# Kernel tuning notes

Hardware: AMD Instinct MI355X
Metric: run time of the kernel (lower is better)

## Reference

```python
import jax, jax.numpy as jnp
import numpy as np

N, E = 100000, 3200000
IN, HID, OUT, EDGE = 32, 32, 32, 8

def _lin(k, fi, fo):
    s = 1.0 / np.sqrt(fi)
    return jax.random.uniform(k, (fi, fo), jnp.float32, -s, s)

def setup_inputs() -> dict:
    key = jax.random.key(0)
    ks = jax.random.split(key, 12)
    return {
        "node_feat": jax.random.normal(ks[0], (N, IN), jnp.float32),
        "coord_feat": jax.random.normal(ks[1], (N, 3), jnp.float32),
        "edge_feat": jax.random.normal(ks[2], (E, EDGE), jnp.float32),
        "src": jax.random.randint(ks[3], (E,), 0, N, jnp.int32),
        "dst": jax.random.randint(ks[4], (E,), 0, N, jnp.int32),
        # edge MLP: Linear(2*IN+EDGE+1 -> HID), SiLU, Linear(HID -> HID), SiLU
        "We1": _lin(ks[5], 2 * IN + EDGE + 1, HID), "be1": jnp.zeros((HID,), jnp.float32),
        "We2": _lin(ks[6], HID, HID), "be2": jnp.zeros((HID,), jnp.float32),
        # node MLP: Linear(IN+HID -> HID), SiLU, Linear(HID -> OUT)
        "Wn1": _lin(ks[7], IN + HID, HID), "bn1": jnp.zeros((HID,), jnp.float32),
        "Wn2": _lin(ks[8], HID, OUT), "bn2": jnp.zeros((OUT,), jnp.float32),
        # coord MLP: Linear(HID -> HID), SiLU, Linear(HID -> 1, bias=False)
        "Wc1": _lin(ks[9], HID, HID), "bc1": jnp.zeros((HID,), jnp.float32),
        "Wc2": _lin(ks[10], HID, 1),
    }

def reference(node_feat, coord_feat, edge_feat, src, dst,
              We1, be1, We2, be2, Wn1, bn1, Wn2, bn2, Wc1, bc1, Wc2):
    silu = jax.nn.silu
    # per-edge coordinate difference and radial feature (DGL EGNNConv math)
    x_diff = coord_feat[src] - coord_feat[dst]                       # [E,3]
    radial = jnp.sum(x_diff * x_diff, axis=-1, keepdims=True)        # [E,1]
    x_diff = x_diff / (jnp.sqrt(radial) + 1e-30)                     # normalized
    # edge MLP on concat(src_h, dst_h, radial, edge_feat)
    f = jnp.concatenate([node_feat[src], node_feat[dst], radial, edge_feat], axis=-1)
    msg_h = silu(silu(f @ We1 + be1) @ We2 + be2)                    # [E,HID]
    # coordinate message (coord MLP scalar gate * normalized diff)
    msg_x = (silu(msg_h @ Wc1 + bc1) @ Wc2) * x_diff                 # [E,3]
    # aggregate: sum for h messages, mean for coord messages (at dst)
    h_neigh = jax.ops.segment_sum(msg_h, dst, num_segments=N)        # [N,HID]
    deg = jax.ops.segment_sum(jnp.ones((E, 1), msg_x.dtype), dst, num_segments=N)
    x_neigh = jax.ops.segment_sum(msg_x, dst, num_segments=N) / jnp.maximum(deg, 1.0)
    # node update
    h = silu(jnp.concatenate([node_feat, h_neigh], axis=-1) @ Wn1 + bn1) @ Wn2 + bn2
    x = coord_feat + x_neigh
    return h, x
```

## Files before the change

kernel.cpp:

```cpp
#include <hip/hip_runtime.h>
#include <math.h>

#define TIN   32
#define THID  32
#define TOUT  32
#define TEDGE 8
#define CHUNK 4
#define MAXDEG 64
#define OVF_CAP 65536

typedef __attribute__((ext_vector_type(8))) short bf16x8;
typedef __attribute__((ext_vector_type(4))) float f32x4;

#define MFMA16(a, b, c) __builtin_amdgcn_mfma_f32_16x16x32_bf16((a), (b), (c), 0, 0, 0)

__device__ __forceinline__ unsigned int cvtpk(float lo, float hi) {
    unsigned int r;
    asm("v_cvt_pk_bf16_f32 %0, %1, %2" : "=v"(r) : "v"(lo), "v"(hi));
    return r;
}

__device__ __forceinline__ float silu_f(float x) {
    float e = __expf(-x);
    return x * __builtin_amdgcn_rcpf(1.0f + e);
}

__device__ __forceinline__ float bflo(unsigned int u) { return __uint_as_float(u << 16); }
__device__ __forceinline__ float bfhi(unsigned int u) { return __uint_as_float(u & 0xFFFF0000u); }

union U4F { unsigned int u[4]; bf16x8 v; };
union U4Q { uint4 q; bf16x8 v; };

__device__ __forceinline__ bf16x8 pack8bf(const float* f) {
    U4F t;
    t.u[0] = cvtpk(f[0], f[1]);
    t.u[1] = cvtpk(f[2], f[3]);
    t.u[2] = cvtpk(f[4], f[5]);
    t.u[3] = cvtpk(f[6], f[7]);
    return t.v;
}

__device__ __forceinline__ bf16x8 load_wT(const float* __restrict__ W, int kbase, int ch, int Kreal) {
    float f[8];
    #pragma unroll
    for (int e = 0; e < 8; ++e) {
        int k = kbase + e;
        f[e] = (k < Kreal) ? W[k * 32 + ch] : 0.0f;
    }
    return pack8bf(f);
}

__device__ __forceinline__ bf16x8 load_wA12(const float* __restrict__ We1,
                                            const float* __restrict__ be1, int g, int ch) {
    float f[8];
    #pragma unroll
    for (int e = 0; e < 8; ++e) f[e] = 0.0f;
    if (g == 0) { f[0] = We1[72 * 32 + ch]; f[1] = be1[ch]; }
    else if (g == 1) {
        #pragma unroll
        for (int e = 0; e < 8; ++e) f[e] = We1[(64 + e) * 32 + ch];
    }
    return pack8bf(f);
}

__global__ __launch_bounds__(256) void conv_node_kernel(
    const float* __restrict__ nf, unsigned int* __restrict__ nb, int total )
{
    int i = blockIdx.x * 256 + threadIdx.x;
    int stride = gridDim.x * 256;
    for (; i < total; i += stride) {
        float2 v = reinterpret_cast<const float2*>(nf)[i];
        nb[i] = cvtpk(v.x, v.y);
    }
}

__global__ __launch_bounds__(256) void conv_coord_kernel(
    const float* __restrict__ c, float4* __restrict__ c4, int N)
{
    int i = blockIdx.x * 256 + threadIdx.x;
    int stride = gridDim.x * 256;
    for (; i < N; i += stride) {
        float4 v;
        v.x = c[3*(size_t)i+0]; v.y = c[3*(size_t)i+1]; v.z = c[3*(size_t)i+2]; v.w = 0.0f;
        c4[i] = v;
    }
}

__global__ __launch_bounds__(256) void record_rank_kernel(
    const int* __restrict__ src,
    const int* __restrict__ dst,
    const float4* __restrict__ coord4,
    const float* __restrict__ edge_feat,
    int* __restrict__ cnt,
    int* __restrict__ ovf,
    uint4* __restrict__ recs,
    int E)
{
    int e = blockIdx.x * 256 + threadIdx.x;
    if (e >= E) return;
    int s = src[e], d = dst[e];
    int rank = atomicAdd(&cnt[d], 1);
    if (rank >= MAXDEG) {
        int o = atomicAdd(&cnt[ (int)0] + 0, 0);
        (void)o;
        int oi = atomicAdd(ovf - 1 + 1 + OVF_CAP, 0);
        (void)oi;
    }
    if (rank < MAXDEG) {
        float4 cs = coord4[s];
        float4 cd = coord4[d];
        float dx0 = cs.x - cd.x, dx1 = cs.y - cd.y, dx2 = cs.z - cd.z;
        float radial = dx0*dx0 + dx1*dx1 + dx2*dx2;
        float invn = __builtin_amdgcn_rcpf(sqrtf(radial) + 1e-30f);
        dx0 *= invn; dx1 *= invn; dx2 *= invn;

        const float4* ep = reinterpret_cast<const float4*>(edge_feat + (size_t)e * TEDGE);
        float4 e0 = ep[0], e1 = ep[1];

        size_t slot = ((size_t)d << 6) + rank;
        uint4 r0, r1;
        r0.x = (unsigned int)s;
        r0.y = cvtpk(dx0, dx1);
        r0.z = cvtpk(dx2, e1.w);
        r0.w = 0u;
        r1.x = cvtpk(radial, e0.x);
        r1.y = cvtpk(e0.y, e0.z);
        r1.z = cvtpk(e0.w, e1.x);
        r1.w = cvtpk(e1.y, e1.z);
        recs[2*slot + 0] = r0;
        recs[2*slot + 1] = r1;
    } else {
        int oi = atomicAdd(&((int*)cnt)[  0 ], 0);
        (void)oi;
    }
}

__global__ __launch_bounds__(256) void noop_kernel(int x) { (void)x; }

__global__ __launch_bounds__(256) void egnn_fused(
    const uint4* __restrict__ node_bf4,
    const uint4* __restrict__ recs,
    const int*  __restrict__ cnt,
    const float* __restrict__ We1,
    const float* __restrict__ be1,
    const float* __restrict__ We2,
    const float* __restrict__ be2,
    const float* __restrict__ Wc1,
    const float* __restrict__ bc1,
    const float* __restrict__ Wc2,
    float4* __restrict__ h_acc4,
    float4* __restrict__ xd4,
    int N)
{
    const int lane = threadIdx.x & 63;
    const int wid  = threadIdx.x >> 6;
    const int r    = lane & 15;
    const int g    = lane >> 4;

    bf16x8 A10[2], A11[2], A12[2], A2[2], A3[2];
    A10[0] = load_wT(We1,      8*g, r,      73);
    A10[1] = load_wT(We1,      8*g, 16 + r, 73);
    A11[0] = load_wT(We1, 32 + 8*g, r,      73);
    A11[1] = load_wT(We1, 32 + 8*g, 16 + r, 73);
    A12[0] = load_wA12(We1, be1, g, r);
    A12[1] = load_wA12(We1, be1, g, 16 + r);
    A2[0] = load_wT(We2, 8*g, r, 32);      A2[1] = load_wT(We2, 8*g, 16 + r, 32);
    A3[0] = load_wT(Wc1, 8*g, r, 32);      A3[1] = load_wT(Wc1, 8*g, 16 + r, 32);

    float be2v[8], bc1v[8], wc2v[8];
    #pragma unroll
    for (int h = 0; h < 2; ++h)
        #pragma unroll
        for (int q = 0; q < 4; ++q) {
            int ch = 16*h + 4*g + q;
            be2v[4*h+q] = be2[ch];
            bc1v[4*h+q] = bc1[ch];
            wc2v[4*h+q] = Wc2[ch];
        }

    const bool Hhi = ((g >> 1) & 1) != 0;
    const int  s0L = 32 * (g & 1) + r;
    const int  s1L = s0L + 16;

    int c0n = (blockIdx.x * 4 + wid) * CHUNK;

    for (int n = c0n; n < c0n + CHUNK && n < N; ++n) {
        int deg = cnt[n];
        int len = deg < MAXDEG ? deg : MAXDEG;
        size_t segbase = ((size_t)n << 6);

        U4Q Bd; Bd.q = node_bf4[(size_t)n * 4 + g];

        float ha0[4] = {0.f,0.f,0.f,0.f}, ha1[4] = {0.f,0.f,0.f,0.f};
        float xa0 = 0.f, xa1 = 0.f, xa2 = 0.f;

        for (int t = 0; t < len; t += 16) {
            int idx = t + r;
            bool valid = idx < len;
            size_t slot = segbase + (valid ? idx : 0);

            uint4 rc = recs[2*slot + (g & 1)];
            int srcv = __shfl((int)rc.x, r, 64);

            U4Q Bs; Bs.q = node_bf4[(size_t)srcv * 4 + g];

            U4F Bk2;
            Bk2.u[0] = 0u; Bk2.u[1] = 0u; Bk2.u[2] = 0u; Bk2.u[3] = 0u;
            if (g == 0) {
                Bk2.u[0] = (rc.z >> 16) | 0x3F800000u;
            } else if (g == 1) {
                Bk2.u[0] = rc.x; Bk2.u[1] = rc.y; Bk2.u[2] = rc.z; Bk2.u[3] = rc.w;
            }

            f32x4 acc0 = {0.f,0.f,0.f,0.f}, acc1 = {0.f,0.f,0.f,0.f};
            acc0 = MFMA16(A10[0], Bs.v,   acc0);
            acc0 = MFMA16(A11[0], Bd.v,   acc0);
            acc0 = MFMA16(A12[0], Bk2.v,  acc0);
            acc1 = MFMA16(A10[1], Bs.v,   acc1);
            acc1 = MFMA16(A11[1], Bd.v,   acc1);
            acc1 = MFMA16(A12[1], Bk2.v,  acc1);

            unsigned int pk0 = cvtpk(silu_f(acc0[0]), silu_f(acc0[1]));
            unsigned int pk1 = cvtpk(silu_f(acc0[2]), silu_f(acc0[3]));
            unsigned int pk2 = cvtpk(silu_f(acc1[0]), silu_f(acc1[1]));
            unsigned int pk3 = cvtpk(silu_f(acc1[2]), silu_f(acc1[3]));

            unsigned int al0 = __shfl(pk0, s0L, 64), al1 = __shfl(pk1, s0L, 64);
            unsigned int ah0 = __shfl(pk2, s0L, 64), ah1 = __shfl(pk3, s0L, 64);
            unsigned int bl0 = __shfl(pk0, s1L, 64), bl1 = __shfl(pk1, s1L, 64);
            unsigned int bh0 = __shfl(pk2, s1L, 64), bh1 = __shfl(pk3, s1L, 64);
            U4F B2u;
            B2u.u[0] = Hhi ? ah0 : al0;  B2u.u[1] = Hhi ? ah1 : al1;
            B2u.u[2] = Hhi ? bh0 : bl0;  B2u.u[3] = Hhi ? bh1 : bl1;

            f32x4 m0, m1;
            #pragma unroll
            for (int q = 0; q < 4; ++q) { m0[q] = be2v[q]; m1[q] = be2v[4+q]; }
            m0 = MFMA16(A2[0], B2u.v, m0);
            m1 = MFMA16(A2[1], B2u.v, m1);

            float vm = valid ? 1.0f : 0.0f;
            float s00 = silu_f(m0[0]) * vm, s01 = silu_f(m0[1]) * vm;
            float s02 = silu_f(m0[2]) * vm, s03 = silu_f(m0[3]) * vm;
            float s10 = silu_f(m1[0]) * vm, s11 = silu_f(m1[1]) * vm;
            float s12 = silu_f(m1[2]) * vm, s13 = silu_f(m1[3]) * vm;

            ha0[0] += s00; ha0[1] += s01; ha0[2] += s02; ha0[3] += s03;
            ha1[0] += s10; ha1[1] += s11; ha1[2] += s12; ha1[3] += s13;

            unsigned int mpk0 = cvtpk(s00, s01);
            unsigned int mpk1 = cvtpk(s02, s03);
            unsigned int mpk2 = cvtpk(s10, s11);
            unsigned int mpk3 = cvtpk(s12, s13);

            unsigned int cl0 = __shfl(mpk0, s0L, 64), cl1 = __shfl(mpk1, s0L, 64);
            unsigned int ch0 = __shfl(mpk2, s0L, 64), ch1 = __shfl(mpk3, s0L, 64);
            unsigned int dl0 = __shfl(mpk0, s1L, 64), dl1 = __shfl(mpk1, s1L, 64);
            unsigned int dh0 = __shfl(mpk2, s1L, 64), dh1 = __shfl(mpk3, s1L, 64);
            U4F B3u;
            B3u.u[0] = Hhi ? ch0 : cl0;  B3u.u[1] = Hhi ? ch1 : cl1;
            B3u.u[2] = Hhi ? dh0 : dl0;  B3u.u[3] = Hhi ? dh1 : dl1;

            f32x4 c0, c1;
            #pragma unroll
            for (int q = 0; q < 4; ++q) { c0[q] = bc1v[q]; c1[q] = bc1v[4+q]; }
            c0 = MFMA16(A3[0], B3u.v, c0);
            c1 = MFMA16(A3[1], B3u.v, c1);

            float gp = 0.0f;
            #pragma unroll
            for (int q = 0; q < 4; ++q) {
                gp = fmaf(silu_f(c0[q]), wc2v[q],   gp);
                gp = fmaf(silu_f(c1[q]), wc2v[4+q], gp);
            }
            gp += __shfl_xor(gp, 16, 64);
            gp += __shfl_xor(gp, 32, 64);

            float xd0 = bflo(rc.y), xd1 = bfhi(rc.y), xd2 = bflo(rc.z);
            xa0 = fmaf(gp * vm, xd0, xa0);
            xa1 = fmaf(gp * vm, xd1, xa1);
            xa2 = fmaf(gp * vm, xd2, xa2);
        }

        #pragma unroll
        for (int off = 1; off < 16; off <<= 1) {
            #pragma unroll
            for (int q = 0; q < 4; ++q) {
                ha0[q] += __shfl_xor(ha0[q], off, 64);
                ha1[q] += __shfl_xor(ha1[q], off, 64);
            }
            xa0 += __shfl_xor(xa0, off, 64);
            xa1 += __shfl_xor(xa1, off, 64);
            xa2 += __shfl_xor(xa2, off, 64);
        }

        if (r == 0) {
            float4 v0; v0.x = ha0[0]; v0.y = ha0[1]; v0.z = ha0[2]; v0.w = ha0[3];
            float4 v1; v1.x = ha1[0]; v1.y = ha1[1]; v1.z = ha1[2]; v1.w = ha1[3];
            h_acc4[(size_t)n * 8 + g]     = v0;
            h_acc4[(size_t)n * 8 + 4 + g] = v1;
            if (g == 0) {
                float4 xv; xv.x = xa0; xv.y = xa1; xv.z = xa2; xv.w = (float)deg;
                xd4[n] = xv;
            }
        }
    }
}

__global__ __launch_bounds__(256) void ovf_scan_kernel(
    const int* __restrict__ dst, const int* __restrict__ cnt,
    int* __restrict__ ovf_cnt, int* __restrict__ ovf, int E)
{
    int e = blockIdx.x * 256 + threadIdx.x;
    int stride = gridDim.x * 256;
    for (; e < E; e += stride) {
        if (cnt[dst[e]] > MAXDEG) {
            int o = atomicAdd(ovf_cnt, 1);
            if (o < OVF_CAP) ovf[o] = e;
        }
    }
}

__global__ __launch_bounds__(64) void ovf_fix_kernel(
    const float* __restrict__ node_feat,
    const float* __restrict__ coord,
    const float* __restrict__ edge_feat,
    const int* __restrict__ src,
    const int* __restrict__ dst,
    const int* __restrict__ ovf_cnt,
    const int* __restrict__ ovf,
    const float* __restrict__ We1,
    const float* __restrict__ be1,
    const float* __restrict__ We2,
    const float* __restrict__ be2,
    const float* __restrict__ Wc1,
    const float* __restrict__ bc1,
    const float* __restrict__ Wc2,
    float* __restrict__ h_acc,
    float4* __restrict__ xd4,
    int E)
{
    int total = *ovf_cnt;
    if (total > OVF_CAP) total = OVF_CAP;
    for (int i = blockIdx.x * 64 + threadIdx.x; i < total; i += gridDim.x * 64) {
        int e = ovf[i];
        int s = src[e], d = dst[e];
        bool first = true;
        for (int j = 0; j < i; ++j) if (dst[ovf[j]] == d) { first = false; break; }
        if (!first) continue;
        float hsum[THID];
        #pragma unroll
        for (int j = 0; j < THID; ++j) hsum[j] = 0.f;
        float xs0 = 0.f, xs1 = 0.f, xs2 = 0.f;
        int degc = 0;
        for (int ee = 0; ee < E; ++ee) {
            if (dst[ee] != d) continue;
            ++degc;
            int ss = src[ee];
            float dx0 = coord[3*(size_t)ss+0] - coord[3*(size_t)d+0];
            float dx1 = coord[3*(size_t)ss+1] - coord[3*(size_t)d+1];
            float dx2 = coord[3*(size_t)ss+2] - coord[3*(size_t)d+2];
            float radial = dx0*dx0 + dx1*dx1 + dx2*dx2;
            float invn = 1.0f / (sqrtf(radial) + 1e-30f);
            dx0 *= invn; dx1 *= invn; dx2 *= invn;
            float f[73];
            for (int k = 0; k < 32; ++k) f[k] = node_feat[(size_t)ss*TIN + k];
            for (int k = 0; k < 32; ++k) f[32+k] = node_feat[(size_t)d*TIN + k];
            f[64] = radial;
            for (int k = 0; k < 8; ++k) f[65+k] = edge_feat[(size_t)ee*TEDGE + k];
            float a1[THID];
            for (int j = 0; j < THID; ++j) a1[j] = be1[j];
            for (int k = 0; k < 73; ++k) {
                float fk = f[k];
                for (int j = 0; j < THID; ++j) a1[j] = fmaf(fk, We1[k*THID + j], a1[j]);
            }
            for (int j = 0; j < THID; ++j) a1[j] = silu_f(a1[j]);
            float msg[THID];
            for (int j = 0; j < THID; ++j) msg[j] = be2[j];
            for (int k = 0; k < THID; ++k) {
                float fk = a1[k];
                for (int j = 0; j < THID; ++j) msg[j] = fmaf(fk, We2[k*THID + j], msg[j]);
            }
            for (int j = 0; j < THID; ++j) msg[j] = silu_f(msg[j]);
            float c1[THID];
            for (int j = 0; j < THID; ++j) c1[j] = bc1[j];
            for (int k = 0; k < THID; ++k) {
                float fk = msg[k];
                for (int j = 0; j < THID; ++j) c1[j] = fmaf(fk, Wc1[k*THID + j], c1[j]);
            }
            float gate = 0.0f;
            for (int j = 0; j < THID; ++j) gate = fmaf(silu_f(c1[j]), Wc2[j], gate);
            for (int j = 0; j < THID; ++j) hsum[j] += msg[j];
            xs0 += gate * dx0; xs1 += gate * dx1; xs2 += gate * dx2;
        }
        for (int j = 0; j < THID; ++j) h_acc[(size_t)d * THID + j] = hsum[j];
        float4 xv; xv.x = xs0; xv.y = xs1; xv.z = xs2; xv.w = (float)degc;
        xd4[d] = xv;
    }
}

__global__ __launch_bounds__(256) void egnn_edge_atomic(
    const float* __restrict__ node_feat,
    const float* __restrict__ coord,
    const float* __restrict__ edge_feat,
    const int*   __restrict__ src,
    const int*   __restrict__ dst,
    const float* __restrict__ We1,
    const float* __restrict__ be1,
    const float* __restrict__ We2,
    const float* __restrict__ be2,
    const float* __restrict__ Wc1,
    const float* __restrict__ bc1,
    const float* __restrict__ Wc2,
    float* __restrict__ h_acc,
    float* __restrict__ x_acc,
    int E)
{
    int e = blockIdx.x * 256 + threadIdx.x;
    if (e >= E) return;
    int s = src[e];
    int d = dst[e];
    float dx0 = coord[3*(size_t)s+0] - coord[3*(size_t)d+0];
    float dx1 = coord[3*(size_t)s+1] - coord[3*(size_t)d+1];
    float dx2 = coord[3*(size_t)s+2] - coord[3*(size_t)d+2];
    float radial = dx0*dx0 + dx1*dx1 + dx2*dx2;
    float invn = 1.0f / (sqrtf(radial) + 1e-30f);
    dx0 *= invn; dx1 *= invn; dx2 *= invn;
    float f[73];
    #pragma unroll
    for (int i = 0; i < 32; ++i) f[i] = node_feat[(size_t)s*TIN + i];
    #pragma unroll
    for (int i = 0; i < 32; ++i) f[32+i] = node_feat[(size_t)d*TIN + i];
    f[64] = radial;
    #pragma unroll
    for (int i = 0; i < 8; ++i) f[65+i] = edge_feat[(size_t)e*TEDGE + i];
    float a1[THID];
    #pragma unroll
    for (int j = 0; j < THID; ++j) a1[j] = be1[j];
    for (int k = 0; k < 73; ++k) {
        float fk = f[k];
        #pragma unroll
        for (int j = 0; j < THID; ++j) a1[j] = fmaf(fk, We1[k*THID + j], a1[j]);
    }
    #pragma unroll
    for (int j = 0; j < THID; ++j) a1[j] = silu_f(a1[j]);
    float msg[THID];
    #pragma unroll
    for (int j = 0; j < THID; ++j) msg[j] = be2[j];
    for (int k = 0; k < THID; ++k) {
        float fk = a1[k];
        #pragma unroll
        for (int j = 0; j < THID; ++j) msg[j] = fmaf(fk, We2[k*THID + j], msg[j]);
    }
    #pragma unroll
    for (int j = 0; j < THID; ++j) msg[j] = silu_f(msg[j]);
    float c1[THID];
    #pragma unroll
    for (int j = 0; j < THID; ++j) c1[j] = bc1[j];
    for (int k = 0; k < THID; ++k) {
        float fk = msg[k];
        #pragma unroll
        for (int j = 0; j < THID; ++j) c1[j] = fmaf(fk, Wc1[k*THID + j], c1[j]);
    }
    float gate = 0.0f;
    #pragma unroll
    for (int j = 0; j < THID; ++j) gate = fmaf(silu_f(c1[j]), Wc2[j], gate);
    float* ha = h_acc + (size_t)d * THID;
    #pragma unroll
    for (int j = 0; j < THID; ++j) atomicAdd(ha + j, msg[j]);
    atomicAdd(x_acc + (size_t)d*4 + 0, gate * dx0);
    atomicAdd(x_acc + (size_t)d*4 + 1, gate * dx1);
    atomicAdd(x_acc + (size_t)d*4 + 2, gate * dx2);
    atomicAdd(x_acc + (size_t)d*4 + 3, 1.0f);
}

__global__ __launch_bounds__(256) void egnn_node(
    const float* __restrict__ node_feat,
    const float* __restrict__ coord,
    const float* __restrict__ Wn1,
    const float* __restrict__ bn1,
    const float* __restrict__ Wn2,
    const float* __restrict__ bn2,
    const float* __restrict__ h_acc,
    const float4* __restrict__ xd4,
    float* __restrict__ out_h,
    float* __restrict__ out_x,
    int N)
{
    int n = blockIdx.x * 256 + threadIdx.x;
    if (n >= N) return;

    float f2[2*TIN];
    {
        const float4* p = reinterpret_cast<const float4*>(node_feat + (size_t)n * TIN);
        #pragma unroll
        for (int i = 0; i < TIN/4; ++i) {
            float4 v = p[i];
            f2[4*i+0]=v.x; f2[4*i+1]=v.y; f2[4*i+2]=v.z; f2[4*i+3]=v.w;
        }
    }
    {
        const float4* p = reinterpret_cast<const float4*>(h_acc + (size_t)n * THID);
        #pragma unroll
        for (int i = 0; i < THID/4; ++i) {
            float4 v = p[i];
            f2[TIN+4*i+0]=v.x; f2[TIN+4*i+1]=v.y; f2[TIN+4*i+2]=v.z; f2[TIN+4*i+3]=v.w;
        }
    }

    float a[THID];
    #pragma unroll
    for (int j = 0; j < THID; ++j) a[j] = bn1[j];
    #pragma unroll
    for (int k = 0; k < 2*TIN; ++k) {
        float fk = f2[k];
        #pragma unroll
        for (int j = 0; j < THID; ++j) a[j] = fmaf(fk, Wn1[k*THID + j], a[j]);
    }
    #pragma unroll
    for (int j = 0; j < THID; ++j) a[j] = silu_f(a[j]);

    float h[TOUT];
    #pragma unroll
    for (int j = 0; j < TOUT; ++j) h[j] = bn2[j];
    #pragma unroll
    for (int k = 0; k < THID; ++k) {
        float fk = a[k];
        #pragma unroll
        for (int j = 0; j < TOUT; ++j) h[j] = fmaf(fk, Wn2[k*TOUT + j], h[j]);
    }

    float4* po = reinterpret_cast<float4*>(out_h + (size_t)n * TOUT);
    #pragma unroll
    for (int i = 0; i < TOUT/4; ++i) {
        float4 v; v.x=h[4*i+0]; v.y=h[4*i+1]; v.z=h[4*i+2]; v.w=h[4*i+3];
        po[i] = v;
    }

    float4 xv = xd4[n];
    float dg = fmaxf(xv.w, 1.0f);
    float inv = __builtin_amdgcn_rcpf(dg);
    out_x[(size_t)n*3+0] = coord[(size_t)n*3+0] + xv.x * inv;
    out_x[(size_t)n*3+1] = coord[(size_t)n*3+1] + xv.y * inv;
    out_x[(size_t)n*3+2] = coord[(size_t)n*3+2] + xv.z * inv;
}

extern "C" void kernel_launch(void* const* d_in, const int* in_sizes, int n_in,
                              void* d_out, int out_size, void* d_ws, size_t ws_size,
                              hipStream_t stream) {
    const float* node_feat = (const float*)d_in[0];
    const float* coord     = (const float*)d_in[1];
    const float* edge_feat = (const float*)d_in[2];
    const int*   src       = (const int*)d_in[3];
    const int*   dst       = (const int*)d_in[4];
    const float* We1 = (const float*)d_in[5];
    const float* be1 = (const float*)d_in[6];
    const float* We2 = (const float*)d_in[7];
    const float* be2 = (const float*)d_in[8];
    const float* Wn1 = (const float*)d_in[9];
    const float* bn1 = (const float*)d_in[10];
    const float* Wn2 = (const float*)d_in[11];
    const float* bn2 = (const float*)d_in[12];
    const float* Wc1 = (const float*)d_in[13];
    const float* bc1 = (const float*)d_in[14];
    const float* Wc2 = (const float*)d_in[15];

    int N = in_sizes[0] / TIN;
    int E = in_sizes[3];

    float* out_h = (float*)d_out;
    float* out_x = out_h + (size_t)N * TOUT;

    uint4*        recs    = (uint4*)d_ws;
    unsigned int* node_bf = (unsigned int*)(recs + ((size_t)N << 6) * 2);
    float4*       coord4  = (float4*)(node_bf + (size_t)N * 16);
    float*        h_acc   = (float*)(coord4 + N);
    float4*       xd4     = (float4*)(h_acc + (size_t)N * THID);
    int*          cnt     = (int*)(xd4 + N);
    int*          ovf     = cnt + (N + 1);
    size_t need = (size_t)((char*)(ovf + OVF_CAP) - (char*)d_ws);

    if (need <= ws_size) {
        conv_node_kernel<<<2048, 256, 0, stream>>>(node_feat, node_bf, N * 16);
        conv_coord_kernel<<<(N + 255) / 256, 256, 0, stream>>>(coord, coord4, N);
        hipMemsetAsync(cnt, 0, (size_t)(N + 1) * 4, stream);
        record_rank_kernel<<<(E + 255) / 256, 256, 0, stream>>>(
            src, dst, coord4, edge_feat, cnt, ovf, recs, E);
        int nchunks = (N + CHUNK - 1) / CHUNK;
        egnn_fused<<<(nchunks + 3) / 4, 256, 0, stream>>>(
            (const uint4*)node_bf, recs, cnt,
            We1, be1, We2, be2, Wc1, bc1, Wc2,
            (float4*)h_acc, xd4, N);
        ovf_scan_kernel<<<256, 256, 0, stream>>>(dst, cnt, cnt + N, ovf, E);
        ovf_fix_kernel<<<8, 64, 0, stream>>>(
            node_feat, coord, edge_feat, src, dst, cnt + N, ovf,
            We1, be1, We2, be2, Wc1, bc1, Wc2, h_acc, xd4, E);
        egnn_node<<<(N + 255) / 256, 256, 0, stream>>>(
            node_feat, coord, Wn1, bn1, Wn2, bn2,
            h_acc, xd4, out_h, out_x, N);
    } else {
        float* fh_acc = (float*)d_ws;
        float* fx_acc = fh_acc + (size_t)N * THID;
        hipMemsetAsync(d_ws, 0, sizeof(float) * (size_t)N * (THID + 4), stream);
        egnn_edge_atomic<<<(E + 255) / 256, 256, 0, stream>>>(
            node_feat, coord, edge_feat, src, dst,
            We1, be1, We2, be2, Wc1, bc1, Wc2,
            fh_acc, fx_acc, E);
        egnn_node<<<(N + 255) / 256, 256, 0, stream>>>(
            node_feat, coord, Wn1, bn1, Wn2, bn2,
            fh_acc, (const float4*)fx_acc, out_h, out_x, N);
    }
}
```

Measured before the change: 493.3 us.

## Split edge records into src and bf16 edge arrays, compute geometry in fused kernel

The rank kernel now writes only the source index and bf16 edge features into separate slot arrays. The fused kernel gathers source coordinates itself to compute the radial term and normalized direction, and it computes the dst-node part of the first layer once per node instead of once per edge tile. This removes the 32-byte packed record writes and the coordinate gathers from the scatter kernel, which should cut scattered write traffic. The overflow scan is replaced by a per-node fix kernel. In exchange the fused kernel adds a random coord gather per edge.

```diff
diff --git a/kernel.cpp b/kernel.cpp
--- a/kernel.cpp
+++ b/kernel.cpp
@@ -7,7 +7,6 @@
 #define TEDGE 8
 #define CHUNK 4
 #define MAXDEG 64
-#define OVF_CAP 65536
 
 typedef __attribute__((ext_vector_type(8))) short bf16x8;
 typedef __attribute__((ext_vector_type(4))) float f32x4;
@@ -24,9 +23,6 @@
     float e = __expf(-x);
     return x * __builtin_amdgcn_rcpf(1.0f + e);
 }
-
-__device__ __forceinline__ float bflo(unsigned int u) { return __uint_as_float(u << 16); }
-__device__ __forceinline__ float bfhi(unsigned int u) { return __uint_as_float(u & 0xFFFF0000u); }
 
 union U4F { unsigned int u[4]; bf16x8 v; };
 union U4Q { uint4 q; bf16x8 v; };
@@ -55,10 +51,10 @@
     float f[8];
     #pragma unroll
     for (int e = 0; e < 8; ++e) f[e] = 0.0f;
-    if (g == 0) { f[0] = We1[72 * 32 + ch]; f[1] = be1[ch]; }
+    if (g == 0) { f[0] = We1[64 * 32 + ch]; f[1] = be1[ch]; }
     else if (g == 1) {
         #pragma unroll
-        for (int e = 0; e < 8; ++e) f[e] = We1[(64 + e) * 32 + ch];
+        for (int e = 0; e < 8; ++e) f[e] = We1[(65 + e) * 32 + ch];
     }
     return pack8bf(f);
 }
@@ -89,57 +85,35 @@
 __global__ __launch_bounds__(256) void record_rank_kernel(
     const int* __restrict__ src,
     const int* __restrict__ dst,
-    const float4* __restrict__ coord4,
     const float* __restrict__ edge_feat,
     int* __restrict__ cnt,
-    int* __restrict__ ovf,
-    uint4* __restrict__ recs,
+    int* __restrict__ srcA,
+    uint4* __restrict__ efA,
     int E)
 {
     int e = blockIdx.x * 256 + threadIdx.x;
     if (e >= E) return;
-    int s = src[e], d = dst[e];
+    int d = dst[e];
     int rank = atomicAdd(&cnt[d], 1);
-    if (rank >= MAXDEG) {
-        int o = atomicAdd(&cnt[ (int)0] + 0, 0);
-        (void)o;
-        int oi = atomicAdd(ovf - 1 + 1 + OVF_CAP, 0);
-        (void)oi;
-    }
-    if (rank < MAXDEG) {
-        float4 cs = coord4[s];
-        float4 cd = coord4[d];
-        float dx0 = cs.x - cd.x, dx1 = cs.y - cd.y, dx2 = cs.z - cd.z;
-        float radial = dx0*dx0 + dx1*dx1 + dx2*dx2;
-        float invn = __builtin_amdgcn_rcpf(sqrtf(radial) + 1e-30f);
-        dx0 *= invn; dx1 *= invn; dx2 *= invn;
-
-        const float4* ep = reinterpret_cast<const float4*>(edge_feat + (size_t)e * TEDGE);
-        float4 e0 = ep[0], e1 = ep[1];
-
-        size_t slot = ((size_t)d << 6) + rank;
-        uint4 r0, r1;
-        r0.x = (unsigned int)s;
-        r0.y = cvtpk(dx0, dx1);
-        r0.z = cvtpk(dx2, e1.w);
-        r0.w = 0u;
-        r1.x = cvtpk(radial, e0.x);
-        r1.y = cvtpk(e0.y, e0.z);
-        r1.z = cvtpk(e0.w, e1.x);
-        r1.w = cvtpk(e1.y, e1.z);
-        recs[2*slot + 0] = r0;
-        recs[2*slot + 1] = r1;
-    } else {
-        int oi = atomicAdd(&((int*)cnt)[  0 ], 0);
-        (void)oi;
-    }
-}
-
-__global__ __launch_bounds__(256) void noop_kernel(int x) { (void)x; }
+    if (rank >= MAXDEG) return;
+    int slot = (d << 6) + rank;
+
+    srcA[slot] = src[e];
+    const float4* ep = reinterpret_cast<const float4*>(edge_feat + (size_t)e * TEDGE);
+    float4 e0 = ep[0], e1 = ep[1];
+    uint4 ef;
+    ef.x = cvtpk(e0.x, e0.y);
+    ef.y = cvtpk(e0.z, e0.w);
+    ef.z = cvtpk(e1.x, e1.y);
+    ef.w = cvtpk(e1.z, e1.w);
+    efA[slot] = ef;
+}
 
 __global__ __launch_bounds__(256) void egnn_fused(
     const uint4* __restrict__ node_bf4,
-    const uint4* __restrict__ recs,
+    const float4* __restrict__ coord4,
+    const int*  __restrict__ srcA,
+    const uint4* __restrict__ efA,
     const int*  __restrict__ cnt,
     const float* __restrict__ We1,
     const float* __restrict__ be1,
@@ -187,9 +161,14 @@
     for (int n = c0n; n < c0n + CHUNK && n < N; ++n) {
         int deg = cnt[n];
         int len = deg < MAXDEG ? deg : MAXDEG;
-        size_t segbase = ((size_t)n << 6);
+        int segbase = n << 6;
 
         U4Q Bd; Bd.q = node_bf4[(size_t)n * 4 + g];
+        float4 cd = coord4[n];
+
+        f32x4 z4 = {0.f,0.f,0.f,0.f};
+        f32x4 dst0 = MFMA16(A11[0], Bd.v, z4);
+        f32x4 dst1 = MFMA16(A11[1], Bd.v, z4);
 
         float ha0[4] = {0.f,0.f,0.f,0.f}, ha1[4] = {0.f,0.f,0.f,0.f};
         float xa0 = 0.f, xa1 = 0.f, xa2 = 0.f;
@@ -197,27 +176,30 @@
         for (int t = 0; t < len; t += 16) {
             int idx = t + r;
             bool valid = idx < len;
-            size_t slot = segbase + (valid ? idx : 0);
-
-            uint4 rc = recs[2*slot + (g & 1)];
-            int srcv = __shfl((int)rc.x, r, 64);
-
+            int slot = segbase + (valid ? idx : 0);
+
+            int srcv = srcA[slot];
             U4Q Bs; Bs.q = node_bf4[(size_t)srcv * 4 + g];
 
+            float dx0 = 0.f, dx1 = 0.f, dx2 = 0.f;
             U4F Bk2;
             Bk2.u[0] = 0u; Bk2.u[1] = 0u; Bk2.u[2] = 0u; Bk2.u[3] = 0u;
             if (g == 0) {
-                Bk2.u[0] = (rc.z >> 16) | 0x3F800000u;
+                float4 cs = coord4[srcv];
+                dx0 = cs.x - cd.x; dx1 = cs.y - cd.y; dx2 = cs.z - cd.z;
+                float radial = dx0*dx0 + dx1*dx1 + dx2*dx2;
+                float invn = __builtin_amdgcn_rcpf(sqrtf(radial) + 1e-30f);
+                dx0 *= invn; dx1 *= invn; dx2 *= invn;
+                Bk2.u[0] = cvtpk(radial, 1.0f);
             } else if (g == 1) {
-                Bk2.u[0] = rc.x; Bk2.u[1] = rc.y; Bk2.u[2] = rc.z; Bk2.u[3] = rc.w;
+                uint4 ef = efA[slot];
+                Bk2.u[0] = ef.x; Bk2.u[1] = ef.y; Bk2.u[2] = ef.z; Bk2.u[3] = ef.w;
             }
 
-            f32x4 acc0 = {0.f,0.f,0.f,0.f}, acc1 = {0.f,0.f,0.f,0.f};
+            f32x4 acc0 = dst0, acc1 = dst1;
             acc0 = MFMA16(A10[0], Bs.v,   acc0);
-            acc0 = MFMA16(A11[0], Bd.v,   acc0);
             acc0 = MFMA16(A12[0], Bk2.v,  acc0);
             acc1 = MFMA16(A10[1], Bs.v,   acc1);
-            acc1 = MFMA16(A11[1], Bd.v,   acc1);
             acc1 = MFMA16(A12[1], Bk2.v,  acc1);
 
             unsigned int pk0 = cvtpk(silu_f(acc0[0]), silu_f(acc0[1]));
@@ -276,10 +258,9 @@
             gp += __shfl_xor(gp, 16, 64);
             gp += __shfl_xor(gp, 32, 64);
 
-            float xd0 = bflo(rc.y), xd1 = bfhi(rc.y), xd2 = bflo(rc.z);
-            xa0 = fmaf(gp * vm, xd0, xa0);
-            xa1 = fmaf(gp * vm, xd1, xa1);
-            xa2 = fmaf(gp * vm, xd2, xa2);
+            xa0 = fmaf(gp * vm, dx0, xa0);
+            xa1 = fmaf(gp * vm, dx1, xa1);
+            xa2 = fmaf(gp * vm, dx2, xa2);
         }
 
         #pragma unroll
@@ -307,28 +288,13 @@
     }
 }
 
-__global__ __launch_bounds__(256) void ovf_scan_kernel(
-    const int* __restrict__ dst, const int* __restrict__ cnt,
-    int* __restrict__ ovf_cnt, int* __restrict__ ovf, int E)
-{
-    int e = blockIdx.x * 256 + threadIdx.x;
-    int stride = gridDim.x * 256;
-    for (; e < E; e += stride) {
-        if (cnt[dst[e]] > MAXDEG) {
-            int o = atomicAdd(ovf_cnt, 1);
-            if (o < OVF_CAP) ovf[o] = e;
-        }
-    }
-}
-
-__global__ __launch_bounds__(64) void ovf_fix_kernel(
+__global__ __launch_bounds__(256) void ovf_fix_node(
     const float* __restrict__ node_feat,
     const float* __restrict__ coord,
     const float* __restrict__ edge_feat,
     const int* __restrict__ src,
     const int* __restrict__ dst,
-    const int* __restrict__ ovf_cnt,
-    const int* __restrict__ ovf,
+    const int* __restrict__ cnt,
     const float* __restrict__ We1,
     const float* __restrict__ be1,
     const float* __restrict__ We2,
@@ -338,65 +304,60 @@
     const float* __restrict__ Wc2,
     float* __restrict__ h_acc,
     float4* __restrict__ xd4,
-    int E)
-{
-    int total = *ovf_cnt;
-    if (total > OVF_CAP) total = OVF_CAP;
-    for (int i = blockIdx.x * 64 + threadIdx.x; i < total; i += gridDim.x * 64) {
-        int e = ovf[i];
-        int s = src[e], d = dst[e];
-        bool first = true;
-        for (int j = 0; j < i; ++j) if (dst[ovf[j]] == d) { first = false; break; }
-        if (!first) continue;
-        float hsum[THID];
-        #pragma unroll
-        for (int j = 0; j < THID; ++j) hsum[j] = 0.f;
-        float xs0 = 0.f, xs1 = 0.f, xs2 = 0.f;
-        int degc = 0;
-        for (int ee = 0; ee < E; ++ee) {
-            if (dst[ee] != d) continue;
-            ++degc;
-            int ss = src[ee];
-            float dx0 = coord[3*(size_t)ss+0] - coord[3*(size_t)d+0];
-            float dx1 = coord[3*(size_t)ss+1] - coord[3*(size_t)d+1];
-            float dx2 = coord[3*(size_t)ss+2] - coord[3*(size_t)d+2];
-            float radial = dx0*dx0 + dx1*dx1 + dx2*dx2;
-            float invn = 1.0f / (sqrtf(radial) + 1e-30f);
-            dx0 *= invn; dx1 *= invn; dx2 *= invn;
-            float f[73];
-            for (int k = 0; k < 32; ++k) f[k] = node_feat[(size_t)ss*TIN + k];
-            for (int k = 0; k < 32; ++k) f[32+k] = node_feat[(size_t)d*TIN + k];
-            f[64] = radial;
-            for (int k = 0; k < 8; ++k) f[65+k] = edge_feat[(size_t)ee*TEDGE + k];
-            float a1[THID];
-            for (int j = 0; j < THID; ++j) a1[j] = be1[j];
-            for (int k = 0; k < 73; ++k) {
-                float fk = f[k];
-                for (int j = 0; j < THID; ++j) a1[j] = fmaf(fk, We1[k*THID + j], a1[j]);
-            }
-            for (int j = 0; j < THID; ++j) a1[j] = silu_f(a1[j]);
-            float msg[THID];
-            for (int j = 0; j < THID; ++j) msg[j] = be2[j];
-            for (int k = 0; k < THID; ++k) {
-                float fk = a1[k];
-                for (int j = 0; j < THID; ++j) msg[j] = fmaf(fk, We2[k*THID + j], msg[j]);
-            }
-            for (int j = 0; j < THID; ++j) msg[j] = silu_f(msg[j]);
-            float c1[THID];
-            for (int j = 0; j < THID; ++j) c1[j] = bc1[j];
-            for (int k = 0; k < THID; ++k) {
-                float fk = msg[k];
-                for (int j = 0; j < THID; ++j) c1[j] = fmaf(fk, Wc1[k*THID + j], c1[j]);
-            }
-            float gate = 0.0f;
-            for (int j = 0; j < THID; ++j) gate = fmaf(silu_f(c1[j]), Wc2[j], gate);
-            for (int j = 0; j < THID; ++j) hsum[j] += msg[j];
-            xs0 += gate * dx0; xs1 += gate * dx1; xs2 += gate * dx2;
-        }
-        for (int j = 0; j < THID; ++j) h_acc[(size_t)d * THID + j] = hsum[j];
-        float4 xv; xv.x = xs0; xv.y = xs1; xv.z = xs2; xv.w = (float)degc;
-        xd4[d] = xv;
-    }
+    int N, int E)
+{
+    int n = blockIdx.x * 256 + threadIdx.x;
+    if (n >= N) return;
+    if (cnt[n] <= MAXDEG) return;
+
+    float hsum[THID];
+    #pragma unroll
+    for (int j = 0; j < THID; ++j) hsum[j] = 0.f;
+    float xs0 = 0.f, xs1 = 0.f, xs2 = 0.f;
+    int degc = 0;
+    for (int ee = 0; ee < E; ++ee) {
+        if (dst[ee] != n) continue;
+        ++degc;
+        int ss = src[ee];
+        float dx0 = coord[3*(size_t)ss+0] - coord[3*(size_t)n+0];
+        float dx1 = coord[3*(size_t)ss+1] - coord[3*(size_t)n+1];
+        float dx2 = coord[3*(size_t)ss+2] - coord[3*(size_t)n+2];
+        float radial = dx0*dx0 + dx1*dx1 + dx2*dx2;
+        float invn = 1.0f / (sqrtf(radial) + 1e-30f);
+        dx0 *= invn; dx1 *= invn; dx2 *= invn;
+        float f[73];
+        for (int k = 0; k < 32; ++k) f[k] = node_feat[(size_t)ss*TIN + k];
+        for (int k = 0; k < 32; ++k) f[32+k] = node_feat[(size_t)n*TIN + k];
+        f[64] = radial;
+        for (int k = 0; k < 8; ++k) f[65+k] = edge_feat[(size_t)ee*TEDGE + k];
+        float a1[THID];
+        for (int j = 0; j < THID; ++j) a1[j] = be1[j];
+        for (int k = 0; k < 73; ++k) {
+            float fk = f[k];
+            for (int j = 0; j < THID; ++j) a1[j] = fmaf(fk, We1[k*THID + j], a1[j]);
+        }
+        for (int j = 0; j < THID; ++j) a1[j] = silu_f(a1[j]);
+        float msg[THID];
+        for (int j = 0; j < THID; ++j) msg[j] = be2[j];
+        for (int k = 0; k < THID; ++k) {
+            float fk = a1[k];
+            for (int j = 0; j < THID; ++j) msg[j] = fmaf(fk, We2[k*THID + j], msg[j]);
+        }
+        for (int j = 0; j < THID; ++j) msg[j] = silu_f(msg[j]);
+        float c1[THID];
+        for (int j = 0; j < THID; ++j) c1[j] = bc1[j];
+        for (int k = 0; k < THID; ++k) {
+            float fk = msg[k];
+            for (int j = 0; j < THID; ++j) c1[j] = fmaf(fk, Wc1[k*THID + j], c1[j]);
+        }
+        float gate = 0.0f;
+        for (int j = 0; j < THID; ++j) gate = fmaf(silu_f(c1[j]), Wc2[j], gate);
+        for (int j = 0; j < THID; ++j) hsum[j] += msg[j];
+        xs0 += gate * dx0; xs1 += gate * dx1; xs2 += gate * dx2;
+    }
+    for (int j = 0; j < THID; ++j) h_acc[(size_t)n * THID + j] = hsum[j];
+    float4 xv; xv.x = xs0; xv.y = xs1; xv.z = xs2; xv.w = (float)degc;
+    xd4[n] = xv;
 }
 
 __global__ __launch_bounds__(256) void egnn_edge_atomic(
@@ -571,30 +532,29 @@
     float* out_h = (float*)d_out;
     float* out_x = out_h + (size_t)N * TOUT;
 
-    uint4*        recs    = (uint4*)d_ws;
-    unsigned int* node_bf = (unsigned int*)(recs + ((size_t)N << 6) * 2);
-    float4*       coord4  = (float4*)(node_bf + (size_t)N * 16);
-    float*        h_acc   = (float*)(coord4 + N);
-    float4*       xd4     = (float4*)(h_acc + (size_t)N * THID);
-    int*          cnt     = (int*)(xd4 + N);
-    int*          ovf     = cnt + (N + 1);
-    size_t need = (size_t)((char*)(ovf + OVF_CAP) - (char*)d_ws);
+    uint4*        efA     = (uint4*)d_ws;
+    float4*       coord4  = (float4*)(efA + ((size_t)N << 6));
+    float4*       xd4     = coord4 + N;
+    float*        h_acc   = (float*)(xd4 + N);
+    unsigned int* node_bf = (unsigned int*)(h_acc + (size_t)N * THID);
+    int*          srcA    = (int*)(node_bf + (size_t)N * 16);
+    int*          cnt     = srcA + ((size_t)N << 6);
+    size_t need = (size_t)((char*)(cnt + N + 1) - (char*)d_ws);
 
     if (need <= ws_size) {
         conv_node_kernel<<<2048, 256, 0, stream>>>(node_feat, node_bf, N * 16);
         conv_coord_kernel<<<(N + 255) / 256, 256, 0, stream>>>(coord, coord4, N);
         hipMemsetAsync(cnt, 0, (size_t)(N + 1) * 4, stream);
         record_rank_kernel<<<(E + 255) / 256, 256, 0, stream>>>(
-            src, dst, coord4, edge_feat, cnt, ovf, recs, E);
+            src, dst, edge_feat, cnt, srcA, efA, E);
         int nchunks = (N + CHUNK - 1) / CHUNK;
         egnn_fused<<<(nchunks + 3) / 4, 256, 0, stream>>>(
-            (const uint4*)node_bf, recs, cnt,
+            (const uint4*)node_bf, coord4, srcA, efA, cnt,
             We1, be1, We2, be2, Wc1, bc1, Wc2,
             (float4*)h_acc, xd4, N);
-        ovf_scan_kernel<<<256, 256, 0, stream>>>(dst, cnt, cnt + N, ovf, E);
-        ovf_fix_kernel<<<8, 64, 0, stream>>>(
-            node_feat, coord, edge_feat, src, dst, cnt + N, ovf,
-            We1, be1, We2, be2, Wc1, bc1, Wc2, h_acc, xd4, E);
+        ovf_fix_node<<<(N + 255) / 256, 256, 0, stream>>>(
+            node_feat, coord, edge_feat, src, dst, cnt,
+            We1, be1, We2, be2, Wc1, bc1, Wc2, h_acc, xd4, N, E);
         egnn_node<<<(N + 255) / 256, 256, 0, stream>>>(
             node_feat, coord, Wn1, bn1, Wn2, bn2,
             h_acc, xd4, out_h, out_x, N);
```

Measured after the change: 520.0 us. 1.05x slower.
